# Optimization experiments

Hardware: AMD Instinct MI355X
Metric: run time of the kernel (lower is better)

## Reference

```python
import jax, jax.numpy as jnp
import numpy as np

PAD_ID, CLS_ID, SEP_ID = 0, 101, 102
B, S, D = 32, 1024, 1024
VOCAB = 30000


def setup_inputs() -> dict:
    key = jax.random.key(0)
    k1, k2, k3, k4, k5 = jax.random.split(key, 5)
    return {
        "hidden_states_src": jax.random.normal(k1, (B, S, D), dtype=jnp.float32),
        "hidden_states_tgt": jax.random.normal(k2, (B, S, D), dtype=jnp.float32),
        "inputs_src": jax.random.randint(k3, (B, S), 0, VOCAB, dtype=jnp.int64),
        "inputs_tgt": jax.random.randint(k4, (B, S), 0, VOCAB, dtype=jnp.int64),
        "guide": jax.random.uniform(k5, (B, 1, S, S), dtype=jnp.float32),
    }


def _special_mask(ids):
    # 1.0 where token is pad/cls/sep (masked out), else 0.0 -- matches torch bool-sum + float()
    m = (ids == PAD_ID) | (ids == CLS_ID) | (ids == SEP_ID)
    return m.astype(jnp.float32)


def reference(hidden_states_src, hidden_states_tgt, inputs_src, inputs_tgt, guide):
    dt = hidden_states_src.dtype
    mask_src = _special_mask(inputs_src)  # [B,S]
    mask_tgt = _special_mask(inputs_tgt)
    len_src = jnp.sum(1.0 - mask_src, axis=-1)  # [B]
    len_tgt = jnp.sum(1.0 - mask_tgt, axis=-1)
    # return_extended_attention_mask(1 - mask): (1 - (1 - mask)) * -10000 = mask * -10000
    ext_src = (mask_src * -10000.0).astype(dt)[:, None, None, :]  # [B,1,1,S]
    ext_tgt = (mask_tgt * -10000.0).astype(dt)[:, None, None, :]
    # single-head QK^T: [B,1,S,S]
    scores = jnp.einsum("bsd,btd->bst", hidden_states_src, hidden_states_tgt)[:, None]
    scores_src = scores + ext_tgt                          # mask invalid tgt keys
    scores_tgt = scores + jnp.swapaxes(ext_src, -1, -2)    # mask invalid src rows, [B,1,S,1] bcast
    probs_src = jax.nn.softmax(scores_src, axis=-1)  # normalize over tgt
    probs_tgt = jax.nn.softmax(scores_tgt, axis=-2)  # normalize over src
    so_src = jnp.sum(probs_src * guide, axis=(-1, -2)).reshape(-1)  # [B]
    so_tgt = jnp.sum(probs_tgt * guide, axis=(-1, -2)).reshape(-1)
    so_loss = -jnp.mean(so_src / len_src + so_tgt / len_tgt)
    return so_loss
```

## Files before the change

### kernel.cpp

```cpp
#include <hip/hip_runtime.h>
#include <stdint.h>

#define Bb 32
#define Ss 1024
#define Dd 1024

typedef __attribute__((ext_vector_type(8))) short short8v;
typedef __attribute__((ext_vector_type(4))) float f32x4;

struct __align__(16) F4 { float v[4]; };

typedef __attribute__((address_space(1))) const void gvoid;
typedef __attribute__((address_space(3))) void svoid;

__device__ inline void gl_lds16(void* lds, const void* g) {
  __builtin_amdgcn_global_load_lds((gvoid*)g, (svoid*)lds, 16, 0, 0);
}

__device__ inline float wredmax(float v) {
#pragma unroll
  for (int o = 32; o > 0; o >>= 1) v = fmaxf(v, __shfl_xor(v, o));
  return v;
}
__device__ inline float wredsum(float v) {
#pragma unroll
  for (int o = 32; o > 0; o >>= 1) v += __shfl_xor(v, o);
  return v;
}

__device__ inline unsigned short f2bf(float f) {
  uint32_t x = __float_as_uint(f);
  uint32_t r = (x + 0x7fffu + ((x >> 16) & 1u)) >> 16;
  return (unsigned short)r;
}

__global__ __launch_bounds__(256) void k_mask(const int* __restrict__ idsS,
                                              const int* __restrict__ idsT,
                                              float* extS, float* extT,
                                              float* invLenS, float* invLenT,
                                              float* wsAcc) {
  const int b = blockIdx.x, tid = threadIdx.x;
  if (b == 0 && tid == 0) wsAcc[0] = 0.0f;
  __shared__ float sh[4];
  for (int side = 0; side < 2; ++side) {
    const int* ids = side ? idsT : idsS;
    float* ext = side ? extT : extS;
    float* il = side ? invLenT : invLenS;
    int cnt = 0;
    for (int i = tid; i < Ss; i += 256) {
      int v = ids[b * Ss + i];
      bool sp = (v == 0) || (v == 101) || (v == 102);
      ext[b * Ss + i] = sp ? -10000.0f : 0.0f;
      cnt += sp ? 0 : 1;
    }
    float c = wredsum((float)cnt);
    if ((tid & 63) == 0) sh[tid >> 6] = c;
    __syncthreads();
    if (tid == 0) il[b] = 1.0f / (sh[0] + sh[1] + sh[2] + sh[3]);
    __syncthreads();
  }
}

__global__ __launch_bounds__(256) void k_cvt(const float* __restrict__ src,
                                             const float* __restrict__ tgt,
                                             unsigned short* __restrict__ srcB,
                                             unsigned short* __restrict__ tgtB) {
  const size_t n = (size_t)Bb * Ss * Dd;
  const size_t units = (2 * n) / 4;
  const size_t stride = (size_t)gridDim.x * blockDim.x;
  for (size_t u = (size_t)blockIdx.x * blockDim.x + threadIdx.x; u < units; u += stride) {
    size_t e = u * 4;
    const float* ip;
    unsigned short* op;
    if (e < n) { ip = src + e; op = srcB + e; }
    else       { ip = tgt + (e - n); op = tgtB + (e - n); }
    F4 x = *(const F4*)ip;
    ushort4 o;
    o.x = f2bf(x.v[0]); o.y = f2bf(x.v[1]); o.z = f2bf(x.v[2]); o.w = f2bf(x.v[3]);
    *(ushort4*)op = o;
  }
}

__global__ __launch_bounds__(256) void k_gemm(const unsigned short* __restrict__ Ag0,
                                              const unsigned short* __restrict__ Bg0,
                                              float* __restrict__ C) {
  __shared__ __align__(16) unsigned short As[128 * 32];
  __shared__ __align__(16) unsigned short Bs[128 * 32];
  const int tile = blockIdx.x, b = blockIdx.y;
  const int tm = tile >> 3, tn = tile & 7;
  const int tid = threadIdx.x, w = tid >> 6, l = tid & 63;
  const int wr = w >> 1, wc = w & 1;
  const int lr = l & 15, lk = (l >> 4) * 8;
  const size_t bb = (size_t)b * (Ss * Dd);
  const unsigned short* Ag = Ag0 + bb + (size_t)(tm * 128) * Dd;
  const unsigned short* Bg = Bg0 + bb + (size_t)(tn * 128) * Dd;
  const int rA = l >> 2, kq = (l & 3) * 8;

  f32x4 acc[4][4];
#pragma unroll
  for (int m = 0; m < 4; ++m)
#pragma unroll
    for (int n = 0; n < 4; ++n) acc[m][n] = (f32x4){0.f, 0.f, 0.f, 0.f};

  for (int kt = 0; kt < Dd / 32; ++kt) {
    const int kb = kt * 32;
    __syncthreads();
#pragma unroll
    for (int i = 0; i < 2; ++i) {
      const int c = w * 2 + i;
      gl_lds16((char*)As + c * 1024, Ag + (size_t)(c * 16 + rA) * Dd + kb + kq);
      gl_lds16((char*)Bs + c * 1024, Bg + (size_t)(c * 16 + rA) * Dd + kb + kq);
    }
    __syncthreads();
    short8v af[4], bf[4];
#pragma unroll
    for (int m = 0; m < 4; ++m)
      af[m] = *(const short8v*)&As[(wr * 64 + m * 16 + lr) * 32 + lk];
#pragma unroll
    for (int n = 0; n < 4; ++n)
      bf[n] = *(const short8v*)&Bs[(wc * 64 + n * 16 + lr) * 32 + lk];
#pragma unroll
    for (int m = 0; m < 4; ++m)
#pragma unroll
      for (int n = 0; n < 4; ++n)
        acc[m][n] = __builtin_amdgcn_mfma_f32_16x16x32_bf16(af[m], bf[n], acc[m][n], 0, 0, 0);
  }

  float* Cb = C + (size_t)b * (Ss * Ss);
  const int r0 = tm * 128 + wr * 64 + (l >> 4) * 4;
  const int c0 = tn * 128 + wc * 64 + lr;
#pragma unroll
  for (int m = 0; m < 4; ++m)
#pragma unroll
    for (int n = 0; n < 4; ++n)
#pragma unroll
      for (int j = 0; j < 4; ++j)
        Cb[(size_t)(r0 + m * 16 + j) * Ss + c0 + n * 16] = acc[m][n][j];
}

__global__ __launch_bounds__(256) void k_stats(const float* __restrict__ scores,
                                               const float* __restrict__ extS,
                                               const float* __restrict__ extT,
                                               float* __restrict__ rowM,
                                               float* __restrict__ rowIS,
                                               float* __restrict__ pcM,
                                               float* __restrict__ pcS) {
  const int sc = blockIdx.x, b = blockIdx.y;
  const int tid = threadIdx.x, w = tid >> 6, l = tid & 63;
  F4 et[4];
  const float* etp = extT + b * Ss;
#pragma unroll
  for (int c = 0; c < 4; ++c) et[c] = *(const F4*)&etp[c * 256 + l * 4];
  float cm[16], cs[16];
#pragma unroll
  for (int i = 0; i < 16; ++i) { cm[i] = -INFINITY; cs[i] = 0.0f; }
  const float* esp = extS + b * Ss;
  const size_t bbase = (size_t)b * (Ss * Ss);

  for (int it = 0; it < 8; ++it) {
    const int s = sc * 32 + it * 4 + w;
    const float* rp = scores + bbase + (size_t)s * Ss;
    F4 x[4];
#pragma unroll
    for (int c = 0; c < 4; ++c) x[c] = *(const F4*)&rp[c * 256 + l * 4];
    const float es = esp[s];
    float rm = -INFINITY;
#pragma unroll
    for (int c = 0; c < 4; ++c)
#pragma unroll
      for (int j = 0; j < 4; ++j) rm = fmaxf(rm, x[c].v[j] + et[c].v[j]);
    rm = wredmax(rm);
    float rs = 0.0f;
#pragma unroll
    for (int c = 0; c < 4; ++c)
#pragma unroll
      for (int j = 0; j < 4; ++j) rs += __expf(x[c].v[j] + et[c].v[j] - rm);
    rs = wredsum(rs);
    if (l == 0) { rowM[b * Ss + s] = rm; rowIS[b * Ss + s] = 1.0f / rs; }
#pragma unroll
    for (int c = 0; c < 4; ++c)
#pragma unroll
      for (int j = 0; j < 4; ++j) {
        const int i = c * 4 + j;
        const float y = x[c].v[j] + es;
        const float ym = fmaxf(cm[i], y);
        cs[i] = cs[i] * __expf(cm[i] - ym) + __expf(y - ym);
        cm[i] = ym;
      }
  }
  const int p = sc * 4 + w;
  float* pm = pcM + ((size_t)b * 128 + p) * Ss;
  float* ps = pcS + ((size_t)b * 128 + p) * Ss;
#pragma unroll
  for (int c = 0; c < 4; ++c) {
    F4 om, os;
#pragma unroll
    for (int j = 0; j < 4; ++j) { om.v[j] = cm[c * 4 + j]; os.v[j] = cs[c * 4 + j]; }
    *(F4*)&pm[c * 256 + l * 4] = om;
    *(F4*)&ps[c * 256 + l * 4] = os;
  }
}

__global__ __launch_bounds__(256) void k_merge(const float* __restrict__ pcM,
                                               const float* __restrict__ pcS,
                                               float* __restrict__ colM,
                                               float* __restrict__ colIS) {
  const int i = blockIdx.x * 256 + threadIdx.x;
  const int b = i >> 10, t = i & 1023;
  const float* pm = pcM + (size_t)b * 128 * Ss + t;
  const float* ps = pcS + (size_t)b * 128 * Ss + t;
  float M = -INFINITY, Sm = 0.0f;
  for (int p = 0; p < 128; ++p) {
    const float m2 = pm[(size_t)p * Ss];
    const float s2 = ps[(size_t)p * Ss];
    const float nm = fmaxf(M, m2);
    Sm = Sm * __expf(M - nm) + s2 * __expf(m2 - nm);
    M = nm;
  }
  colM[i] = M;
  colIS[i] = 1.0f / Sm;
}

__global__ __launch_bounds__(256) void k_wsum(const float* __restrict__ scores,
                                              const float* __restrict__ guide,
                                              const float* __restrict__ rowM,
                                              const float* __restrict__ rowIS,
                                              const float* __restrict__ colM,
                                              const float* __restrict__ colIS,
                                              const float* __restrict__ extS,
                                              const float* __restrict__ extT,
                                              const float* __restrict__ invLenS,
                                              const float* __restrict__ invLenT,
                                              float* __restrict__ wsAcc) {
  const size_t units = (size_t)Bb * Ss * (Ss / 4);
  const size_t stride = (size_t)gridDim.x * blockDim.x;
  float acc = 0.0f;
  for (size_t u = (size_t)blockIdx.x * blockDim.x + threadIdx.x; u < units; u += stride) {
    const int tq = (int)(u & 255);
    const int s = (int)((u >> 8) & 1023);
    const int b = (int)(u >> 18);
    const size_t ro = ((size_t)b * Ss + s) * Ss + tq * 4;
    F4 sc4 = *(const F4*)(scores + ro);
    F4 g4 = *(const F4*)(guide + ro);
    const int bs = b * Ss + s;
    const float rm = rowM[bs], irs = rowIS[bs], es = extS[bs];
    const float ils = invLenS[b], ilt = invLenT[b];
    const int bt = b * Ss + tq * 4;
    F4 et4 = *(const F4*)(extT + bt);
    F4 cm4 = *(const F4*)(colM + bt);
    F4 ic4 = *(const F4*)(colIS + bt);
#pragma unroll
    for (int j = 0; j < 4; ++j) {
      const float psrc = __expf(sc4.v[j] + et4.v[j] - rm) * irs * ils;
      const float ptgt = __expf(sc4.v[j] + es - cm4.v[j]) * ic4.v[j] * ilt;
      acc += (psrc + ptgt) * g4.v[j];
    }
  }
  acc = wredsum(acc);
  __shared__ float sh[4];
  if ((threadIdx.x & 63) == 0) sh[threadIdx.x >> 6] = acc;
  __syncthreads();
  if (threadIdx.x == 0) atomicAdd(wsAcc, sh[0] + sh[1] + sh[2] + sh[3]);
}

__global__ void k_final(const float* __restrict__ wsAcc, float* __restrict__ out) {
  out[0] = -wsAcc[0] / (float)Bb;
}

extern "C" void kernel_launch(void* const* d_in, const int* in_sizes, int n_in,
                              void* d_out, int out_size, void* d_ws, size_t ws_size,
                              hipStream_t stream) {
  const float* hsrc = (const float*)d_in[0];
  const float* htgt = (const float*)d_in[1];
  const int* isrc = (const int*)d_in[2];
  const int* itgt = (const int*)d_in[3];
  const float* guide = (const float*)d_in[4];
  float* out = (float*)d_out;

  const size_t n = (size_t)Bb * Ss * Dd;
  char* w = (char*)d_ws;
  size_t off = 0;
  auto alloc = [&](size_t bytes) -> void* {
    void* p = (void*)(w + off);
    off += (bytes + 255) & ~(size_t)255;
    return p;
  };
  unsigned short* srcB = (unsigned short*)alloc(n * 2);
  unsigned short* tgtB = (unsigned short*)alloc(n * 2);
  float* scores = (float*)alloc((size_t)Bb * Ss * Ss * 4);
  float* extS  = (float*)alloc((size_t)Bb * Ss * 4);
  float* extT  = (float*)alloc((size_t)Bb * Ss * 4);
  float* rowM  = (float*)alloc((size_t)Bb * Ss * 4);
  float* rowIS = (float*)alloc((size_t)Bb * Ss * 4);
  float* colM  = (float*)alloc((size_t)Bb * Ss * 4);
  float* colIS = (float*)alloc((size_t)Bb * Ss * 4);
  float* invLenS = (float*)alloc(Bb * 4);
  float* invLenT = (float*)alloc(Bb * 4);
  float* wsAcc = (float*)alloc(256);
  float* pcM = (float*)alloc((size_t)Bb * 128 * Ss * 4);
  float* pcS = (float*)alloc((size_t)Bb * 128 * Ss * 4);

  k_mask<<<Bb, 256, 0, stream>>>(isrc, itgt, extS, extT, invLenS, invLenT, wsAcc);
  k_cvt<<<4096, 256, 0, stream>>>(hsrc, htgt, srcB, tgtB);
  k_gemm<<<dim3(64, Bb), 256, 0, stream>>>(srcB, tgtB, scores);
  k_stats<<<dim3(32, Bb), 256, 0, stream>>>(scores, extS, extT, rowM, rowIS, pcM, pcS);
  k_merge<<<128, 256, 0, stream>>>(pcM, pcS, colM, colIS);
  k_wsum<<<2048, 256, 0, stream>>>(scores, guide, rowM, rowIS, colM, colIS,
                                   extS, extT, invLenS, invLenT, wsAcc);
  k_final<<<1, 1, 0, stream>>>(wsAcc, out);
}
```

Baseline: 587.8 us.

## Widen GEMM K-tile with swizzled LDS, vectorize stores, merge column partials in-block

The GEMM now stages 64-wide K slices in LDS with an XOR swizzle to avoid bank conflicts. It swaps the MFMA operands so each lane holds four contiguous output columns, which lets it store them with one 16-byte write. The conversion kernel processes 8 elements per thread with a 16-byte store. The stats kernel merges its four warps' column partials through shared memory before writing, which cuts the partial buffer and the merge loop from 128 to 32 entries per column. Costs are more LDS per GEMM block and an added block barrier plus shared memory in the stats kernel.

```diff
diff --git a/kernel.cpp b/kernel.cpp
--- a/kernel.cpp
+++ b/kernel.cpp
@@ -66,35 +66,41 @@
                                              unsigned short* __restrict__ srcB,
                                              unsigned short* __restrict__ tgtB) {
   const size_t n = (size_t)Bb * Ss * Dd;
-  const size_t units = (2 * n) / 4;
+  const size_t units = (2 * n) / 8;
   const size_t stride = (size_t)gridDim.x * blockDim.x;
   for (size_t u = (size_t)blockIdx.x * blockDim.x + threadIdx.x; u < units; u += stride) {
-    size_t e = u * 4;
+    size_t e = u * 8;
     const float* ip;
     unsigned short* op;
     if (e < n) { ip = src + e; op = srcB + e; }
     else       { ip = tgt + (e - n); op = tgtB + (e - n); }
-    F4 x = *(const F4*)ip;
-    ushort4 o;
-    o.x = f2bf(x.v[0]); o.y = f2bf(x.v[1]); o.z = f2bf(x.v[2]); o.w = f2bf(x.v[3]);
-    *(ushort4*)op = o;
+    F4 x0 = *(const F4*)ip;
+    F4 x1 = *(const F4*)(ip + 4);
+    union { unsigned short u16[8]; short8v v; } o;
+#pragma unroll
+    for (int j = 0; j < 4; ++j) {
+      o.u16[j] = f2bf(x0.v[j]);
+      o.u16[4 + j] = f2bf(x1.v[j]);
+    }
+    *(short8v*)op = o.v;
   }
 }
 
 __global__ __launch_bounds__(256) void k_gemm(const unsigned short* __restrict__ Ag0,
                                               const unsigned short* __restrict__ Bg0,
                                               float* __restrict__ C) {
-  __shared__ __align__(16) unsigned short As[128 * 32];
-  __shared__ __align__(16) unsigned short Bs[128 * 32];
+  __shared__ __align__(16) unsigned short As[128 * 64];
+  __shared__ __align__(16) unsigned short Bs[128 * 64];
   const int tile = blockIdx.x, b = blockIdx.y;
   const int tm = tile >> 3, tn = tile & 7;
   const int tid = threadIdx.x, w = tid >> 6, l = tid & 63;
   const int wr = w >> 1, wc = w & 1;
-  const int lr = l & 15, lk = (l >> 4) * 8;
+  const int lr = l & 15;
   const size_t bb = (size_t)b * (Ss * Dd);
   const unsigned short* Ag = Ag0 + bb + (size_t)(tm * 128) * Dd;
   const unsigned short* Bg = Bg0 + bb + (size_t)(tn * 128) * Dd;
-  const int rA = l >> 2, kq = (l & 3) * 8;
+  const int srow = l >> 3;
+  const int skslot = (l & 7) ^ srow;
 
   f32x4 acc[4][4];
 #pragma unroll
@@ -102,40 +108,46 @@
 #pragma unroll
     for (int n = 0; n < 4; ++n) acc[m][n] = (f32x4){0.f, 0.f, 0.f, 0.f};
 
-  for (int kt = 0; kt < Dd / 32; ++kt) {
-    const int kb = kt * 32;
+  for (int kt = 0; kt < Dd / 64; ++kt) {
+    const int kb = kt * 64;
     __syncthreads();
 #pragma unroll
-    for (int i = 0; i < 2; ++i) {
-      const int c = w * 2 + i;
-      gl_lds16((char*)As + c * 1024, Ag + (size_t)(c * 16 + rA) * Dd + kb + kq);
-      gl_lds16((char*)Bs + c * 1024, Bg + (size_t)(c * 16 + rA) * Dd + kb + kq);
+    for (int i = 0; i < 4; ++i) {
+      const int c = w * 4 + i;
+      gl_lds16((char*)As + c * 1024, Ag + (size_t)(c * 8 + srow) * Dd + kb + skslot * 8);
+      gl_lds16((char*)Bs + c * 1024, Bg + (size_t)(c * 8 + srow) * Dd + kb + skslot * 8);
     }
     __syncthreads();
-    short8v af[4], bf[4];
-#pragma unroll
-    for (int m = 0; m < 4; ++m)
-      af[m] = *(const short8v*)&As[(wr * 64 + m * 16 + lr) * 32 + lk];
+#pragma unroll
+    for (int kk = 0; kk < 2; ++kk) {
+      const int ks = kk * 4 + (l >> 4);
+      short8v af[4], bf[4];
+#pragma unroll
+      for (int m = 0; m < 4; ++m) {
+        const int row = wr * 64 + m * 16 + lr;
+        af[m] = *(const short8v*)&As[row * 64 + ((ks ^ (row & 7)) * 8)];
+      }
+#pragma unroll
+      for (int n = 0; n < 4; ++n) {
+        const int row = wc * 64 + n * 16 + lr;
+        bf[n] = *(const short8v*)&Bs[row * 64 + ((ks ^ (row & 7)) * 8)];
+      }
+#pragma unroll
+      for (int m = 0; m < 4; ++m)
+#pragma unroll
+        for (int n = 0; n < 4; ++n)
+          acc[m][n] = __builtin_amdgcn_mfma_f32_16x16x32_bf16(bf[n], af[m], acc[m][n], 0, 0, 0);
+    }
+  }
+
+  float* Cb = C + (size_t)b * (Ss * Ss);
+  const int sr0 = tm * 128 + wr * 64 + lr;
+  const int tc0 = tn * 128 + wc * 64 + (l >> 4) * 4;
+#pragma unroll
+  for (int m = 0; m < 4; ++m)
 #pragma unroll
     for (int n = 0; n < 4; ++n)
-      bf[n] = *(const short8v*)&Bs[(wc * 64 + n * 16 + lr) * 32 + lk];
-#pragma unroll
-    for (int m = 0; m < 4; ++m)
-#pragma unroll
-      for (int n = 0; n < 4; ++n)
-        acc[m][n] = __builtin_amdgcn_mfma_f32_16x16x32_bf16(af[m], bf[n], acc[m][n], 0, 0, 0);
-  }
-
-  float* Cb = C + (size_t)b * (Ss * Ss);
-  const int r0 = tm * 128 + wr * 64 + (l >> 4) * 4;
-  const int c0 = tn * 128 + wc * 64 + lr;
-#pragma unroll
-  for (int m = 0; m < 4; ++m)
-#pragma unroll
-    for (int n = 0; n < 4; ++n)
-#pragma unroll
-      for (int j = 0; j < 4; ++j)
-        Cb[(size_t)(r0 + m * 16 + j) * Ss + c0 + n * 16] = acc[m][n][j];
+      *(f32x4*)&Cb[(size_t)(sr0 + m * 16) * Ss + tc0 + n * 16] = acc[m][n];
 }
 
 __global__ __launch_bounds__(256) void k_stats(const float* __restrict__ scores,
@@ -147,6 +159,7 @@
                                                float* __restrict__ pcS) {
   const int sc = blockIdx.x, b = blockIdx.y;
   const int tid = threadIdx.x, w = tid >> 6, l = tid & 63;
+  __shared__ float smM[3][1024], smS[3][1024];
   F4 et[4];
   const float* etp = extT + b * Ss;
 #pragma unroll
@@ -188,16 +201,40 @@
         cm[i] = ym;
       }
   }
-  const int p = sc * 4 + w;
-  float* pm = pcM + ((size_t)b * 128 + p) * Ss;
-  float* ps = pcS + ((size_t)b * 128 + p) * Ss;
-#pragma unroll
-  for (int c = 0; c < 4; ++c) {
-    F4 om, os;
-#pragma unroll
-    for (int j = 0; j < 4; ++j) { om.v[j] = cm[c * 4 + j]; os.v[j] = cs[c * 4 + j]; }
-    *(F4*)&pm[c * 256 + l * 4] = om;
-    *(F4*)&ps[c * 256 + l * 4] = os;
+  if (w > 0) {
+#pragma unroll
+    for (int c = 0; c < 4; ++c) {
+      F4 om, os;
+#pragma unroll
+      for (int j = 0; j < 4; ++j) { om.v[j] = cm[c * 4 + j]; os.v[j] = cs[c * 4 + j]; }
+      *(F4*)&smM[w - 1][c * 256 + l * 4] = om;
+      *(F4*)&smS[w - 1][c * 256 + l * 4] = os;
+    }
+  }
+  __syncthreads();
+  if (w == 0) {
+    float* pm = pcM + ((size_t)b * 32 + sc) * Ss;
+    float* ps = pcS + ((size_t)b * 32 + sc) * Ss;
+#pragma unroll
+    for (int c = 0; c < 4; ++c) {
+      F4 om, os;
+#pragma unroll
+      for (int j = 0; j < 4; ++j) {
+        const int i = c * 4 + j;
+        const int col = c * 256 + l * 4 + j;
+        float M = cm[i], Sm = cs[i];
+#pragma unroll
+        for (int q = 0; q < 3; ++q) {
+          const float m2 = smM[q][col], s2 = smS[q][col];
+          const float nm = fmaxf(M, m2);
+          Sm = Sm * __expf(M - nm) + s2 * __expf(m2 - nm);
+          M = nm;
+        }
+        om.v[j] = M; os.v[j] = Sm;
+      }
+      *(F4*)&pm[c * 256 + l * 4] = om;
+      *(F4*)&ps[c * 256 + l * 4] = os;
+    }
   }
 }
 
@@ -207,10 +244,11 @@
                                                float* __restrict__ colIS) {
   const int i = blockIdx.x * 256 + threadIdx.x;
   const int b = i >> 10, t = i & 1023;
-  const float* pm = pcM + (size_t)b * 128 * Ss + t;
-  const float* ps = pcS + (size_t)b * 128 * Ss + t;
+  const float* pm = pcM + (size_t)b * 32 * Ss + t;
+  const float* ps = pcS + (size_t)b * 32 * Ss + t;
   float M = -INFINITY, Sm = 0.0f;
-  for (int p = 0; p < 128; ++p) {
+#pragma unroll 4
+  for (int p = 0; p < 32; ++p) {
     const float m2 = pm[(size_t)p * Ss];
     const float s2 = ps[(size_t)p * Ss];
     const float nm = fmaxf(M, m2);
@@ -297,8 +335,8 @@
   float* invLenS = (float*)alloc(Bb * 4);
   float* invLenT = (float*)alloc(Bb * 4);
   float* wsAcc = (float*)alloc(256);
-  float* pcM = (float*)alloc((size_t)Bb * 128 * Ss * 4);
-  float* pcS = (float*)alloc((size_t)Bb * 128 * Ss * 4);
+  float* pcM = (float*)alloc((size_t)Bb * 32 * Ss * 4);
+  float* pcS = (float*)alloc((size_t)Bb * 32 * Ss * 4);
 
   k_mask<<<Bb, 256, 0, stream>>>(isrc, itgt, extS, extT, invLenS, invLenT, wsAcc);
   k_cvt<<<4096, 256, 0, stream>>>(hsrc, htgt, srcB, tgtB);
```

Result: faster. 550.6 us (-6.3%).
